# Kernel optimization log

Hardware: AMD Instinct MI355X
Metric: run time of the kernel (lower is better)

## Reference

```python
import jax, jax.numpy as jnp
import numpy as np

N_NODES = 50000
N_EDGES = 800000
IN_DIM = 128
HID = 256
NUM_GRAPHS = 128


def setup_inputs() -> dict:
    key = jax.random.key(0)
    ks = jax.random.split(key, 12)
    x = jax.random.normal(ks[0], (N_NODES, IN_DIM), dtype=jnp.float32)
    edge_index = jax.random.randint(ks[1], (2, N_EDGES), 0, N_NODES, dtype=jnp.int32)
    batch = jnp.sort(jax.random.randint(ks[2], (N_NODES,), 0, NUM_GRAPHS, dtype=jnp.int32))
    def glorot(k, fan_in, fan_out):
        s = jnp.sqrt(6.0 / (fan_in + fan_out))
        return jax.random.uniform(k, (fan_in, fan_out), jnp.float32, -s, s)
    W1 = glorot(ks[3], IN_DIM, HID); b1 = jnp.zeros((HID,), jnp.float32)
    W2 = glorot(ks[4], HID, HID);    b2 = jnp.zeros((HID,), jnp.float32)
    W3 = glorot(ks[5], HID, HID // 2); b3 = jnp.zeros((HID // 2,), jnp.float32)
    W4 = glorot(ks[6], HID // 2, 1);   b4 = jnp.zeros((1,), jnp.float32)
    return {"x": x, "edge_index": edge_index, "batch": batch,
            "W1": W1, "b1": b1, "W2": W2, "b2": b2,
            "W3": W3, "b3": b3, "W4": W4, "b4": b4}


def _gcn_conv(x, src, dst, dinv, W, b, n_nodes):
    # x: [N, F_in] -> [N, F_out]; PyG GCNConv: xW gathered at src, scaled by
    # symmetric norm deg^-1/2[src]*deg^-1/2[dst], scatter-added at dst, + bias.
    h = x @ W                                   # [N, F_out]
    norm = dinv[src] * dinv[dst]                # [E+N]
    msg = h[src] * norm[:, None]                # [E+N, F_out]
    return jax.ops.segment_sum(msg, dst, num_segments=n_nodes) + b


def reference(x, edge_index, batch, W1, b1, W2, b2, W3, b3, W4, b4):
    n = x.shape[0]
    loop = jnp.arange(n, dtype=edge_index.dtype)
    src = jnp.concatenate([edge_index[0], loop])   # add self-loops
    dst = jnp.concatenate([edge_index[1], loop])
    deg = jax.ops.segment_sum(jnp.ones(src.shape[0], x.dtype), dst, num_segments=n)
    dinv = jnp.where(deg > 0, jax.lax.rsqrt(jnp.maximum(deg, 1.0)), 0.0)

    h1 = jax.nn.relu(_gcn_conv(x, src, dst, dinv, W1, b1, n))
    h2 = jax.nn.relu(_gcn_conv(h1, src, dst, dinv, W2, b2, n))

    # global_mean_pool over graph ids
    sums = jax.ops.segment_sum(h2, batch, num_segments=NUM_GRAPHS)          # [G, H]
    cnts = jax.ops.segment_sum(jnp.ones(n, h2.dtype), batch, num_segments=NUM_GRAPHS)
    g = sums / jnp.maximum(cnts, 1.0)[:, None]

    # classifier: Linear->ReLU->(Dropout eval=identity)->Linear->Sigmoid
    z = jax.nn.relu(g @ W3 + b3)
    return jax.nn.sigmoid(z @ W4 + b4)            # [G, 1]
```

## Files before the change

kernel.cpp:

```cpp
#include <hip/hip_runtime.h>
#include <math.h>

#define HID 256
#define INDIM 128
#define NPASS 8

typedef short s16x8 __attribute__((ext_vector_type(8)));
typedef float f32x4 __attribute__((ext_vector_type(4)));
typedef float f32x2 __attribute__((ext_vector_type(2)));

static __device__ __forceinline__ unsigned short f2bf(float f) {
    unsigned int u = __float_as_uint(f);
    unsigned int r = (u + 0x7fffu + ((u >> 16) & 1u)) >> 16;
    return (unsigned short)r;
}

#define DECW(a, base, w)                                                  \
    do {                                                                  \
        f32x2 p0 = __builtin_amdgcn_cvt_pk_f32_fp8((int)(w), false);      \
        f32x2 p1 = __builtin_amdgcn_cvt_pk_f32_fp8((int)(w), true);       \
        a[(base) + 0] += p0[0]; a[(base) + 1] += p0[1];                   \
        a[(base) + 2] += p1[0]; a[(base) + 3] += p1[1];                   \
    } while (0)
#define DEC16(a, u)                                                       \
    do { DECW(a, 0, (u).x); DECW(a, 4, (u).y);                            \
         DECW(a, 8, (u).z); DECW(a, 12, (u).w); } while (0)

__global__ void k_count(const int* __restrict__ dst, int E, int* cnt) {
    int e = blockIdx.x * blockDim.x + threadIdx.x;
    if (e < E) atomicAdd(&cnt[dst[e]], 1);
}

__global__ __launch_bounds__(256) void k_scan_block(const int* __restrict__ cnt,
                                                    int* excl_tmp, int* blksum, int n) {
    __shared__ int sm[256];
    int t = threadIdx.x;
    int i = blockIdx.x * 256 + t;
    int c = (i < n) ? cnt[i] : 0;
    sm[t] = c;
    __syncthreads();
    for (int off = 1; off < 256; off <<= 1) {
        int v = (t >= off) ? sm[t - off] : 0;
        __syncthreads();
        sm[t] += v;
        __syncthreads();
    }
    if (i < n) excl_tmp[i] = sm[t] - c;
    if (t == 255) blksum[blockIdx.x] = sm[255];
}

__global__ __launch_bounds__(256) void k_scan_top(int* blksum, int nb) {
    __shared__ int sm[256];
    int t = threadIdx.x;
    int c = (t < nb) ? blksum[t] : 0;
    sm[t] = c;
    __syncthreads();
    for (int off = 1; off < 256; off <<= 1) {
        int v = (t >= off) ? sm[t - off] : 0;
        __syncthreads();
        sm[t] += v;
        __syncthreads();
    }
    if (t < nb) blksum[t] = sm[t] - c;
}

__global__ __launch_bounds__(256) void k_finalize_rows(const int* __restrict__ excl_tmp,
                                                       const int* __restrict__ blksum,
                                                       const int* __restrict__ cnt,
                                                       int* row_start, int* cursor,
                                                       float* dinv, int n, int E) {
    int i = blockIdx.x * 256 + threadIdx.x;
    if (i < n) {
        int r = excl_tmp[i] + blksum[blockIdx.x];
        row_start[i] = r;
        cursor[i] = r;
        dinv[i] = rsqrtf((float)(cnt[i] + 1));
    }
    if (i == 0) row_start[n] = E;
}

__global__ void k_fill(const int* __restrict__ src, const int* __restrict__ dst,
                       int E, int* cursor, int* __restrict__ csr_src, int n) {
    int e0 = blockIdx.x * blockDim.x + threadIdx.x;
    int stride = gridDim.x * blockDim.x;
    int range = (n + NPASS - 1) / NPASS;
#pragma unroll 1
    for (int p = 0; p < NPASS; p++) {
        int lo = p * range;
        int hi = lo + range;
        for (int e = e0; e < E; e += stride) {
            int d = dst[e];
            if (d >= lo && d < hi) {
                int pos = atomicAdd(&cursor[d], 1);
                csr_src[pos] = src[e];
            }
        }
    }
}

__global__ void k_cast_q(const float* __restrict__ x, const float* __restrict__ dinv,
                         unsigned int* __restrict__ out, int nw) {
    int i = blockIdx.x * blockDim.x + threadIdx.x;
    if (i < nw) {
        float dv = dinv[i >> 5];
        float4 v = ((const float4*)x)[i];
        int w0 = __builtin_amdgcn_cvt_pk_fp8_f32(v.x * dv, v.y * dv, 0, false);
        w0 = __builtin_amdgcn_cvt_pk_fp8_f32(v.z * dv, v.w * dv, w0, true);
        out[i] = (unsigned int)w0;
    }
}

template <int K>
__global__ void k_wtf(const float* __restrict__ W, uint4* __restrict__ Wfrag) {
    constexpr int NK = K / 32;
    int c_tile = blockIdx.x / NK;
    int kk = blockIdx.x % NK;
    int lane = threadIdx.x;
    int c = c_tile * 16 + (lane & 15);
    int k0 = kk * 32 + (lane >> 4) * 8;
    unsigned short b[8];
#pragma unroll
    for (int j = 0; j < 8; j++) b[j] = f2bf(W[(size_t)(k0 + j) * HID + c]);
    uint4 o;
    o.x = (unsigned int)b[0] | ((unsigned int)b[1] << 16);
    o.y = (unsigned int)b[2] | ((unsigned int)b[3] << 16);
    o.z = (unsigned int)b[4] | ((unsigned int)b[5] << 16);
    o.w = (unsigned int)b[6] | ((unsigned int)b[7] << 16);
    Wfrag[(size_t)(c_tile * NK + kk) * 64 + lane] = o;
}

template <int K, int EPI>
__global__ __launch_bounds__(256) void k_gemm_mfma(const unsigned short* __restrict__ Xb,
                                                   const uint4* __restrict__ Wfrag,
                                                   const float* __restrict__ epi,
                                                   void* __restrict__ Yout, int n) {
    constexpr int NK = K / 32;
    __shared__ uint4 bl[4 * NK * 64];

    const int nb = blockIdx.x & 3;
    const int mb = blockIdx.x >> 2;
    const int r0 = mb * 128;
    const int w = threadIdx.x >> 6;
    const int lane = threadIdx.x & 63;
    const int ar = lane & 15;
    const int ak = (lane >> 4) * 8;

    {
        const uint4* gsrc = Wfrag + (size_t)nb * 4 * NK * 64;
        for (int i = threadIdx.x; i < 4 * NK * 64; i += 256) bl[i] = gsrc[i];
    }

    int arow[2];
#pragma unroll
    for (int rt = 0; rt < 2; rt++) {
        int r = r0 + w * 32 + rt * 16 + ar;
        arow[rt] = (r < n) ? r : n - 1;
    }

    f32x4 acc[2][4];
#pragma unroll
    for (int rt = 0; rt < 2; rt++)
#pragma unroll
        for (int ct = 0; ct < 4; ct++) acc[rt][ct] = f32x4{0, 0, 0, 0};

    __syncthreads();

    s16x8 a_cur[2], a_nxt[2];
#pragma unroll
    for (int rt = 0; rt < 2; rt++)
        a_cur[rt] = *(const s16x8*)(Xb + (size_t)arow[rt] * K + ak);

#pragma unroll
    for (int kk = 0; kk < NK; kk++) {
        if (kk + 1 < NK) {
#pragma unroll
            for (int rt = 0; rt < 2; rt++)
                a_nxt[rt] = *(const s16x8*)(Xb + (size_t)arow[rt] * K + (kk + 1) * 32 + ak);
        }
        s16x8 bfrag[4];
#pragma unroll
        for (int ct = 0; ct < 4; ct++)
            bfrag[ct] = ((const s16x8*)bl)[(ct * NK + kk) * 64 + lane];
#pragma unroll
        for (int rt = 0; rt < 2; rt++)
#pragma unroll
            for (int ct = 0; ct < 4; ct++)
                acc[rt][ct] = __builtin_amdgcn_mfma_f32_16x16x32_bf16(a_cur[rt], bfrag[ct],
                                                                      acc[rt][ct], 0, 0, 0);
#pragma unroll
        for (int rt = 0; rt < 2; rt++) a_cur[rt] = a_nxt[rt];
    }

#pragma unroll
    for (int rt = 0; rt < 2; rt++) {
        int rbase = r0 + w * 32 + rt * 16 + (lane >> 4) * 4;
        if constexpr (EPI == 1) {
            unsigned short* Yb = (unsigned short*)Yout;
#pragma unroll
            for (int ct = 0; ct < 4; ct++) {
                int c = nb * 64 + ct * 16 + ar;
                float bc = epi[c];
#pragma unroll
                for (int j = 0; j < 4; j++) {
                    int r = rbase + j;
                    if (r < n) Yb[(size_t)r * HID + c] = f2bf(fmaxf(acc[rt][ct][j] + bc, 0.0f));
                }
            }
        } else {
            unsigned char* Yq = (unsigned char*)Yout;
            float dv[4];
#pragma unroll
            for (int j = 0; j < 4; j++) dv[j] = (rbase + j < n) ? epi[rbase + j] : 0.0f;
#pragma unroll
            for (int ct = 0; ct < 4; ct++) {
                int c = nb * 64 + ct * 16 + ar;
#pragma unroll
                for (int j = 0; j < 4; j++) {
                    int r = rbase + j;
                    if (r < n) {
                        float f = acc[rt][ct][j] * dv[j];
                        int e = __builtin_amdgcn_cvt_pk_fp8_f32(f, f, 0, false);
                        Yq[(size_t)r * HID + c] = (unsigned char)(e & 0xff);
                    }
                }
            }
        }
    }
}

template <int D, bool BIASRELU>
__global__ __launch_bounds__(256) void k_agg_q(const unsigned char* __restrict__ Hq,
                                               const float* __restrict__ dinv,
                                               const int* __restrict__ row_start,
                                               const int* __restrict__ csr_src,
                                               const float* __restrict__ bias,
                                               unsigned short* __restrict__ O, int n) {
    constexpr int LPR = D / 16;
    constexpr int EPW = 64 / LPR;
    const int v = blockIdx.x * 4 + (threadIdx.x >> 6);
    const int lane = threadIdx.x & 63;
    const int sub = lane / LPR;
    const int li = lane % LPR;
    if (v >= n) return;
    const uint4* H4 = (const uint4*)Hq;
    float a[16];
#pragma unroll
    for (int k = 0; k < 16; k++) a[k] = 0.f;
    const int beg = row_start[v], end = row_start[v + 1];
    int i = beg + sub;
    for (; i + 3 * EPW < end; i += 4 * EPW) {
        int s0 = csr_src[i];
        int s1 = csr_src[i + EPW];
        int s2 = csr_src[i + 2 * EPW];
        int s3 = csr_src[i + 3 * EPW];
        uint4 u0 = H4[(size_t)s0 * LPR + li];
        uint4 u1 = H4[(size_t)s1 * LPR + li];
        uint4 u2 = H4[(size_t)s2 * LPR + li];
        uint4 u3 = H4[(size_t)s3 * LPR + li];
        DEC16(a, u0); DEC16(a, u1); DEC16(a, u2); DEC16(a, u3);
    }
    for (; i < end; i += EPW) {
        uint4 u = H4[(size_t)csr_src[i] * LPR + li];
        DEC16(a, u);
    }
#pragma unroll
    for (int off = LPR; off < 64; off <<= 1)
#pragma unroll
        for (int k = 0; k < 16; k++) a[k] += __shfl_xor(a[k], off);

    if (lane < LPR) {
        uint4 us = H4[(size_t)v * LPR + li];
        DEC16(a, us);
        float dv = dinv[v];
        float o[16];
        if constexpr (BIASRELU) {
            const float4* B4 = (const float4*)bias;
#pragma unroll
            for (int q = 0; q < 4; q++) {
                float4 bb = B4[li * 4 + q];
                o[q * 4 + 0] = fmaxf(fmaf(dv, a[q * 4 + 0], bb.x), 0.f);
                o[q * 4 + 1] = fmaxf(fmaf(dv, a[q * 4 + 1], bb.y), 0.f);
                o[q * 4 + 2] = fmaxf(fmaf(dv, a[q * 4 + 2], bb.z), 0.f);
                o[q * 4 + 3] = fmaxf(fmaf(dv, a[q * 4 + 3], bb.w), 0.f);
            }
        } else {
#pragma unroll
            for (int k = 0; k < 16; k++) o[k] = dv * a[k];
        }
        uint4 ow0, ow1;
        ow0.x = (unsigned int)f2bf(o[0]) | ((unsigned int)f2bf(o[1]) << 16);
        ow0.y = (unsigned int)f2bf(o[2]) | ((unsigned int)f2bf(o[3]) << 16);
        ow0.z = (unsigned int)f2bf(o[4]) | ((unsigned int)f2bf(o[5]) << 16);
        ow0.w = (unsigned int)f2bf(o[6]) | ((unsigned int)f2bf(o[7]) << 16);
        ow1.x = (unsigned int)f2bf(o[8]) | ((unsigned int)f2bf(o[9]) << 16);
        ow1.y = (unsigned int)f2bf(o[10]) | ((unsigned int)f2bf(o[11]) << 16);
        ow1.z = (unsigned int)f2bf(o[12]) | ((unsigned int)f2bf(o[13]) << 16);
        ow1.w = (unsigned int)f2bf(o[14]) | ((unsigned int)f2bf(o[15]) << 16);
        uint4* Op = (uint4*)O + (size_t)v * (2 * LPR) + li * 2;
        Op[0] = ow0;
        Op[1] = ow1;
    }
}

#define BFLO(x) __uint_as_float((x) << 16)
#define BFHI(x) __uint_as_float((x) & 0xffff0000u)
#define ACC8(a, u)                                  \
    do {                                            \
        a[0] += BFLO((u).x); a[1] += BFHI((u).x);   \
        a[2] += BFLO((u).y); a[3] += BFHI((u).y);   \
        a[4] += BFLO((u).z); a[5] += BFHI((u).z);   \
        a[6] += BFLO((u).w); a[7] += BFHI((u).w);   \
    } while (0)

__global__ __launch_bounds__(256) void k_pool(const unsigned short* __restrict__ Hb,
                                              const int* __restrict__ batch,
                                              int n, float* __restrict__ G) {
    int g = blockIdx.x;
    int w = threadIdx.x >> 6;
    int lane = threadIdx.x & 63;
    int sub = lane >> 5;
    int li = lane & 31;
    int lo = 0, hi = n;
    while (lo < hi) { int m = (lo + hi) >> 1; if (batch[m] < g) lo = m + 1; else hi = m; }
    int start = lo;
    hi = n;
    while (lo < hi) { int m = (lo + hi) >> 1; if (batch[m] <= g) lo = m + 1; else hi = m; }
    int end = lo;
    const uint4* H4 = (const uint4*)Hb;
    float a[8] = {0, 0, 0, 0, 0, 0, 0, 0};
    for (int v = start + w * 2 + sub; v < end; v += 8) {
        uint4 u = H4[(size_t)v * 32 + li];
        ACC8(a, u);
    }
#pragma unroll
    for (int k = 0; k < 8; k++) a[k] += __shfl_xor(a[k], 32);
    __shared__ float red[4][32][8];
    if (lane < 32) {
#pragma unroll
        for (int k = 0; k < 8; k++) red[w][li][k] = a[k];
    }
    __syncthreads();
    if (w == 0 && lane < 32) {
        float inv = 1.0f / fmaxf((float)(end - start), 1.0f);
        float o[8];
#pragma unroll
        for (int k = 0; k < 8; k++)
            o[k] = (red[0][li][k] + red[1][li][k] + red[2][li][k] + red[3][li][k]) * inv;
        float4* Gp = (float4*)(G + (size_t)g * HID + li * 8);
        Gp[0] = make_float4(o[0], o[1], o[2], o[3]);
        Gp[1] = make_float4(o[4], o[5], o[6], o[7]);
    }
}

__global__ __launch_bounds__(128) void k_cls(const float* __restrict__ G,
                                             const float* __restrict__ W3,
                                             const float* __restrict__ b3,
                                             const float* __restrict__ W4,
                                             const float* __restrict__ b4,
                                             float* __restrict__ out) {
    __shared__ float gr[256];
    __shared__ float red[2];
    int g = blockIdx.x, t = threadIdx.x;
    gr[t] = G[g * 256 + t];
    gr[t + 128] = G[g * 256 + t + 128];
    __syncthreads();
    float z = b3[t];
    for (int k = 0; k < 256; k++) z += gr[k] * W3[k * 128 + t];
    z = fmaxf(z, 0.0f);
    float p = z * W4[t];
    for (int off = 32; off; off >>= 1) p += __shfl_down(p, off);
    if ((t & 63) == 0) red[t >> 6] = p;
    __syncthreads();
    if (t == 0) {
        float tot = red[0] + red[1] + b4[0];
        out[g] = 1.0f / (1.0f + expf(-tot));
    }
}

extern "C" void kernel_launch(void* const* d_in, const int* in_sizes, int n_in,
                              void* d_out, int out_size, void* d_ws, size_t ws_size,
                              hipStream_t stream) {
    const float* x  = (const float*)d_in[0];
    const int*   ei = (const int*)d_in[1];
    const int*   batch = (const int*)d_in[2];
    const float* W1 = (const float*)d_in[3];
    const float* b1 = (const float*)d_in[4];
    const float* W2 = (const float*)d_in[5];
    const float* b2 = (const float*)d_in[6];
    const float* W3 = (const float*)d_in[7];
    const float* b3 = (const float*)d_in[8];
    const float* W4 = (const float*)d_in[9];
    const float* b4 = (const float*)d_in[10];

    const int N = in_sizes[2];
    const int E = in_sizes[1] / 2;
    const int G = out_size;
    const int NB = (N + 255) / 256;

    char* w = (char*)d_ws;
    float* dinv      = (float*)w;  w += ((size_t)N * 4 + 255) & ~(size_t)255;
    int*   cnt       = (int*)w;    w += ((size_t)N * 4 + 255) & ~(size_t)255;
    int*   excl_tmp  = (int*)w;    w += ((size_t)N * 4 + 255) & ~(size_t)255;
    int*   blksum    = (int*)w;    w += 256 * 4;
    int*   row_start = (int*)w;    w += ((size_t)(N + 1) * 4 + 255) & ~(size_t)255;
    int*   cursor    = (int*)w;    w += ((size_t)N * 4 + 255) & ~(size_t)255;
    int*   csr_src   = (int*)w;    w += ((size_t)E * 4 + 255) & ~(size_t)255;
    unsigned char*  xq   = (unsigned char*)w;   w += ((size_t)N * INDIM + 255) & ~(size_t)255;
    unsigned char*  Hq   = (unsigned char*)w;   w += ((size_t)N * HID + 255) & ~(size_t)255;
    uint4* wf1 = (uint4*)w;  w += ((size_t)INDIM * HID * 2 + 255) & ~(size_t)255;
    uint4* wf2 = (uint4*)w;  w += ((size_t)HID * HID * 2 + 255) & ~(size_t)255;
    unsigned short* bufA = (unsigned short*)w;  w += (size_t)N * INDIM * 2;
    unsigned short* bufB = (unsigned short*)w;  w += (size_t)N * HID * 2;
    float* gbuf      = (float*)w;  w += (size_t)G * HID * 4;

    const int* src = ei;
    const int* dst = ei + E;

    k_wtf<INDIM><<<16 * (INDIM / 32), 64, 0, stream>>>(W1, wf1);
    k_wtf<HID><<<16 * (HID / 32), 64, 0, stream>>>(W2, wf2);

    hipMemsetAsync(cnt, 0, (size_t)N * 4, stream);
    k_count<<<(E + 255) / 256, 256, 0, stream>>>(dst, E, cnt);
    k_scan_block<<<NB, 256, 0, stream>>>(cnt, excl_tmp, blksum, N);
    k_scan_top<<<1, 256, 0, stream>>>(blksum, NB);
    k_finalize_rows<<<NB, 256, 0, stream>>>(excl_tmp, blksum, cnt, row_start, cursor, dinv, N, E);
    k_fill<<<(E + 255) / 256, 256, 0, stream>>>(src, dst, E, cursor, csr_src, N);

    int nw = N * INDIM / 4;
    k_cast_q<<<(nw + 255) / 256, 256, 0, stream>>>(x, dinv, (unsigned int*)xq, nw);

    const int gemm_blocks = ((N + 127) / 128) * 4;
    const int agg_blocks  = (N + 3) / 4;

    k_agg_q<INDIM, false><<<agg_blocks, 256, 0, stream>>>(xq, dinv, row_start, csr_src, nullptr, bufA, N);
    k_gemm_mfma<INDIM, 1><<<gemm_blocks, 256, 0, stream>>>(bufA, wf1, b1, bufB, N);

    k_gemm_mfma<HID, 2><<<gemm_blocks, 256, 0, stream>>>(bufB, wf2, dinv, Hq, N);
    k_agg_q<HID, true><<<agg_blocks, 256, 0, stream>>>(Hq, dinv, row_start, csr_src, b2, bufB, N);

    k_pool<<<G, 256, 0, stream>>>(bufB, batch, N, gbuf);
    k_cls<<<G, 128, 0, stream>>>(gbuf, W3, b3, W4, b4, (float*)d_out);
}
```

Baseline: 272.2 us.

## Split wide aggregation across waves and broadcast CSR indices via shuffles

The aggregation kernel now always uses 8 lanes per row segment of 128 features. The 256-wide layer gets two waves per node, each covering half the columns, which doubles wave-level parallelism and lets more neighbours be processed at once. Neighbour indices are loaded once per 64-edge chunk, one per lane, and broadcast with __shfl instead of each lane group reading csr_src itself. The trade-off is that each wave in the second layer re-reads the same index list, and the cost per node grows with the extra shuffles.

After: 309.7 us. 13.8% more time.

```diff
diff --git a/kernel.cpp b/kernel.cpp
--- a/kernel.cpp
+++ b/kernel.cpp
@@ -235,41 +235,61 @@
                                                const int* __restrict__ csr_src,
                                                const float* __restrict__ bias,
                                                unsigned short* __restrict__ O, int n) {
-    constexpr int LPR = D / 16;
-    constexpr int EPW = 64 / LPR;
-    const int v = blockIdx.x * 4 + (threadIdx.x >> 6);
+    constexpr int WPN = D / 128;
+    constexpr int RS = D / 16;
+    const int gwave = blockIdx.x * 4 + (threadIdx.x >> 6);
+    const int v = gwave / WPN;
+    const int woff = gwave & (WPN - 1);
     const int lane = threadIdx.x & 63;
-    const int sub = lane / LPR;
-    const int li = lane % LPR;
+    const int sub = lane >> 3;
+    const int li = lane & 7;
     if (v >= n) return;
     const uint4* H4 = (const uint4*)Hq;
+    const int cbase = woff * 8 + li;
+
     float a[16];
 #pragma unroll
     for (int k = 0; k < 16; k++) a[k] = 0.f;
+
     const int beg = row_start[v], end = row_start[v + 1];
-    int i = beg + sub;
-    for (; i + 3 * EPW < end; i += 4 * EPW) {
-        int s0 = csr_src[i];
-        int s1 = csr_src[i + EPW];
-        int s2 = csr_src[i + 2 * EPW];
-        int s3 = csr_src[i + 3 * EPW];
-        uint4 u0 = H4[(size_t)s0 * LPR + li];
-        uint4 u1 = H4[(size_t)s1 * LPR + li];
-        uint4 u2 = H4[(size_t)s2 * LPR + li];
-        uint4 u3 = H4[(size_t)s3 * LPR + li];
-        DEC16(a, u0); DEC16(a, u1); DEC16(a, u2); DEC16(a, u3);
-    }
-    for (; i < end; i += EPW) {
-        uint4 u = H4[(size_t)csr_src[i] * LPR + li];
-        DEC16(a, u);
-    }
-#pragma unroll
-    for (int off = LPR; off < 64; off <<= 1)
+    for (int base = beg; base < end; base += 64) {
+        int cnt = end - base; if (cnt > 64) cnt = 64;
+        int gi = base + lane; if (gi >= end) gi = end - 1;
+        int idx = csr_src[gi];
+        int e = sub;
+        for (; e + 24 < cnt; e += 32) {
+            int s0 = __shfl(idx, e);
+            int s1 = __shfl(idx, e + 8);
+            int s2 = __shfl(idx, e + 16);
+            int s3 = __shfl(idx, e + 24);
+            uint4 u0 = H4[(size_t)s0 * RS + cbase];
+            uint4 u1 = H4[(size_t)s1 * RS + cbase];
+            uint4 u2 = H4[(size_t)s2 * RS + cbase];
+            uint4 u3 = H4[(size_t)s3 * RS + cbase];
+            DEC16(a, u0); DEC16(a, u1); DEC16(a, u2); DEC16(a, u3);
+        }
+        if (e + 8 < cnt) {
+            int s0 = __shfl(idx, e);
+            int s1 = __shfl(idx, e + 8);
+            uint4 u0 = H4[(size_t)s0 * RS + cbase];
+            uint4 u1 = H4[(size_t)s1 * RS + cbase];
+            DEC16(a, u0); DEC16(a, u1);
+            e += 16;
+        }
+        if (e < cnt) {
+            int s0 = __shfl(idx, e);
+            uint4 u0 = H4[(size_t)s0 * RS + cbase];
+            DEC16(a, u0);
+        }
+    }
+
+#pragma unroll
+    for (int off = 8; off < 64; off <<= 1)
 #pragma unroll
         for (int k = 0; k < 16; k++) a[k] += __shfl_xor(a[k], off);
 
-    if (lane < LPR) {
-        uint4 us = H4[(size_t)v * LPR + li];
+    if (lane < 8) {
+        uint4 us = H4[(size_t)v * RS + cbase];
         DEC16(a, us);
         float dv = dinv[v];
         float o[16];
@@ -277,7 +297,7 @@
             const float4* B4 = (const float4*)bias;
 #pragma unroll
             for (int q = 0; q < 4; q++) {
-                float4 bb = B4[li * 4 + q];
+                float4 bb = B4[woff * 32 + li * 4 + q];
                 o[q * 4 + 0] = fmaxf(fmaf(dv, a[q * 4 + 0], bb.x), 0.f);
                 o[q * 4 + 1] = fmaxf(fmaf(dv, a[q * 4 + 1], bb.y), 0.f);
                 o[q * 4 + 2] = fmaxf(fmaf(dv, a[q * 4 + 2], bb.z), 0.f);
@@ -296,7 +316,7 @@
         ow1.y = (unsigned int)f2bf(o[10]) | ((unsigned int)f2bf(o[11]) << 16);
         ow1.z = (unsigned int)f2bf(o[12]) | ((unsigned int)f2bf(o[13]) << 16);
         ow1.w = (unsigned int)f2bf(o[14]) | ((unsigned int)f2bf(o[15]) << 16);
-        uint4* Op = (uint4*)O + (size_t)v * (2 * LPR) + li * 2;
+        uint4* Op = (uint4*)O + (size_t)v * (D / 8) + (size_t)(woff * 8 + li) * 2;
         Op[0] = ow0;
         Op[1] = ow1;
     }
@@ -430,13 +450,14 @@
     k_cast_q<<<(nw + 255) / 256, 256, 0, stream>>>(x, dinv, (unsigned int*)xq, nw);
 
     const int gemm_blocks = ((N + 127) / 128) * 4;
-    const int agg_blocks  = (N + 3) / 4;
-
-    k_agg_q<INDIM, false><<<agg_blocks, 256, 0, stream>>>(xq, dinv, row_start, csr_src, nullptr, bufA, N);
+    const int agg1_blocks = (N + 3) / 4;
+    const int agg2_blocks = (2 * N + 3) / 4;
+
+    k_agg_q<INDIM, false><<<agg1_blocks, 256, 0, stream>>>(xq, dinv, row_start, csr_src, nullptr, bufA, N);
     k_gemm_mfma<INDIM, 1><<<gemm_blocks, 256, 0, stream>>>(bufA, wf1, b1, bufB, N);
 
     k_gemm_mfma<HID, 2><<<gemm_blocks, 256, 0, stream>>>(bufB, wf2, dinv, Hq, N);
-    k_agg_q<HID, true><<<agg_blocks, 256, 0, stream>>>(Hq, dinv, row_start, csr_src, b2, bufB, N);
+    k_agg_q<HID, true><<<agg2_blocks, 256, 0, stream>>>(Hq, dinv, row_start, csr_src, b2, bufB, N);
 
     k_pool<<<G, 256, 0, stream>>>(bufB, batch, N, gbuf);
     k_cls<<<G, 128, 0, stream>>>(gbuf, W3, b3, W4, b4, (float*)d_out);
```
